# Kernel tuning notes

Hardware: AMD Instinct MI355X
Metric: run time of the kernel (lower is better)

## Reference

```python
import jax, jax.numpy as jnp
import numpy as np

N, L, S, D = 2, 4800, 4800, 256
H0, W0, H1, W1 = 60, 80, 60, 80  # hw0_c, hw1_c (L = H0*W0, S = H1*W1)
THR = 0.2
TEMP = 0.1           # dsmax_temperature
BORDER = 2           # border_rm
INF = 1e9


def setup_inputs() -> dict:
    key = jax.random.key(0)
    k0, k1, k2, k3 = jax.random.split(key, 4)
    feat_c0 = jax.random.normal(k0, (N, L, D), jnp.float32)
    feat_c1 = jax.random.normal(k1, (N, S, D), jnp.float32)
    # final_proj params (Linear(256, 256, bias=True)); scaled like typical init
    W = jax.random.normal(k2, (D, D), jnp.float32) / np.sqrt(D)
    b = jax.random.normal(k3, (D,), jnp.float32) * 0.01
    mask_c0 = jnp.ones((N, L), dtype=bool)
    mask_c1 = jnp.ones((N, S), dtype=bool)
    return {"feat_c0": feat_c0, "feat_c1": feat_c1, "W": W, "b": b,
            "mask_c0": mask_c0, "mask_c1": mask_c1}


def _border_valid(h, w, bd):
    # flattened (h*w,) bool: True away from all four borders (mask_border with v=False)
    r = jnp.arange(h * w)
    hh, ww = r // w, r % w
    return (hh >= bd) & (hh < h - bd) & (ww >= bd) & (ww < w - bd)


def reference(feat_c0, feat_c1, W, b, mask_c0, mask_c1):
    inv_sqrt_d = 1.0 / jnp.sqrt(jnp.asarray(D, jnp.float32))
    # final_proj + 1/sqrt(C) scaling
    f0 = (feat_c0 @ W.T + b) * inv_sqrt_d   # [N, L, D]
    f1 = (feat_c1 @ W.T + b) * inv_sqrt_d   # [N, S, D]
    # pairwise similarity / temperature, masked_fill(-INF) on padded pairs
    sim = jnp.einsum('nlc,nsc->nls', f0, f1) / TEMP   # [N, L, S]
    valid = mask_c0[:, :, None] & mask_c1[:, None, :]
    sim = jnp.where(valid, sim, -INF)
    # dual softmax
    conf_0_to_1 = jax.nn.softmax(sim, axis=2)
    conf_1_to_0 = jax.nn.softmax(sim, axis=1)
    # mutual nearest-neighbour + threshold mask
    m01 = (conf_0_to_1 > THR) & (conf_0_to_1 == conf_0_to_1.max(axis=2, keepdims=True))
    m10 = (conf_1_to_0 > THR) & (conf_1_to_0 == conf_1_to_0.max(axis=1, keepdims=True))
    match_mask = m01 | m10
    # border removal (mask_border with v=False on the [b,h0,w0,h1,w1] view)
    match_mask = (match_mask
                  & _border_valid(H0, W0, BORDER)[None, :, None]
                  & _border_valid(H1, W1, BORDER)[None, None, :])
    # dense form of mconf = max(conf01, conf10) at selected matches
    mconf = jnp.maximum(conf_0_to_1, conf_1_to_0) * match_mask
    return conf_0_to_1, conf_1_to_0, match_mask, mconf
```

## Files before the change

### kernel.cpp

```cpp
#include <hip/hip_runtime.h>

#define LL   4800
#define SSZ  4800
#define DD   256
#define LP   4864
#define NBAT 2

typedef __bf16 bf16x8 __attribute__((ext_vector_type(8)));
typedef float  f32x4  __attribute__((ext_vector_type(4)));

__device__ __forceinline__ unsigned short f2bf(float x) {
  unsigned u = __float_as_uint(x);
  u += 0x7FFFu + ((u >> 16) & 1u);
  return (unsigned short)(u >> 16);
}
__device__ __forceinline__ float bf2f(unsigned short h) {
  return __uint_as_float(((unsigned)h) << 16);
}
__device__ __forceinline__ void gl_lds16(const void* g, void* lds) {
  __builtin_amdgcn_global_load_lds(
      (const __attribute__((address_space(1))) void*)g,
      (__attribute__((address_space(3))) void*)lds, 16, 0, 0);
}
__device__ __forceinline__ bool border_ok(int idx) {
  const int h = idx / 80, w = idx % 80;
  return (h >= 2) && (h < 58) && (w >= 2) && (w < 78);
}
__device__ __forceinline__ void sim_block_decode(int wgid, int& bxs, int& byl, int& bz) {
  const int logical = (wgid & 7) * 361 + (wgid >> 3);
  bz = logical / 1444;
  const int rem = logical - bz * 1444;
  byl = rem / 38;
  bxs = rem - byl * 38;
}

#define F4_FEAT 614400
#define F4_TOT  (F4_FEAT * 2 + 16384)
__global__ void k_convert_all(const float* __restrict__ f0, const float* __restrict__ f1,
                              const float* __restrict__ Wm,
                              unsigned short* __restrict__ fc0hi, unsigned short* __restrict__ fc0lo,
                              unsigned short* __restrict__ fc1hi, unsigned short* __restrict__ fc1lo,
                              unsigned short* __restrict__ Whi,  unsigned short* __restrict__ Wlo) {
  int i = blockIdx.x * blockDim.x + threadIdx.x;
  if (i >= F4_TOT) return;
  const float* src;
  unsigned short *hi, *lo;
  int off;
  if (i < F4_FEAT)          { src = f0; hi = fc0hi; lo = fc0lo; off = i; }
  else if (i < 2 * F4_FEAT) { src = f1; hi = fc1hi; lo = fc1lo; off = i - F4_FEAT; }
  else                      { src = Wm; hi = Whi;  lo = Wlo;  off = i - 2 * F4_FEAT; }
  float4 v = reinterpret_cast<const float4*>(src)[off];
  float xs[4] = {v.x, v.y, v.z, v.w};
  unsigned short hs[4], ls[4];
#pragma unroll
  for (int j = 0; j < 4; ++j) {
    unsigned short h = f2bf(xs[j]);
    hs[j] = h;
    ls[j] = f2bf(xs[j] - bf2f(h));
  }
  ushort4 ho; ho.x = hs[0]; ho.y = hs[1]; ho.z = hs[2]; ho.w = hs[3];
  ushort4 lov; lov.x = ls[0]; lov.y = ls[1]; lov.z = ls[2]; lov.w = ls[3];
  reinterpret_cast<ushort4*>(hi)[off] = ho;
  reinterpret_cast<ushort4*>(lo)[off] = lov;
}

__global__ __launch_bounds__(256, 2)
void k_gemm_proj(const unsigned short* __restrict__ fc0hi, const unsigned short* __restrict__ fc0lo,
                 const unsigned short* __restrict__ fc1hi, const unsigned short* __restrict__ fc1lo,
                 const unsigned short* __restrict__ Whi,  const unsigned short* __restrict__ Wlo,
                 const float* __restrict__ bias,
                 unsigned short* __restrict__ f0h, unsigned short* __restrict__ f1h) {
  extern __shared__ unsigned char smem[];
  unsigned char* sAhi = smem;
  unsigned char* sAlo = smem + 16384;
  unsigned char* sBhi = smem + 32768;
  unsigned char* sBlo = smem + 49152;

  const int t = threadIdx.x;
  const int lane = t & 63, wave = t >> 6;
  const int wr = wave >> 1, wc = wave & 1;
  const int l15 = lane & 15, g4 = lane >> 4;
  const int tr = t >> 3, tch = t & 7;
  const int chg = tch ^ (tr & 7);

  const int mtile = blockIdx.x, ntile = blockIdx.y, tz = blockIdx.z;
  const int nb = (mtile >= 38) ? 1 : 0;
  const int ltile = mtile - nb * 38;

  const unsigned short* Fhi = tz ? fc1hi : fc0hi;
  const unsigned short* Flo = tz ? fc1lo : fc0lo;
  unsigned short* Oh = tz ? f1h : f0h;

  f32x4 acc[4][4] = {};

  for (int kt = 0; kt < DD / 64; ++kt) {
#pragma unroll
    for (int i = 0; i < 4; ++i) {
      const int r = i * 32 + tr;
      const int lrow = ltile * 128 + r;
      const int srcRow = nb * LL + min(lrow, LL - 1);
      const size_t aoff = (size_t)srcRow * DD + kt * 64 + chg * 8;
      const size_t boff = (size_t)(ntile * 128 + r) * DD + kt * 64 + chg * 8;
      const int ldsoff = i * 4096 + t * 16;
      gl_lds16(Fhi + aoff, sAhi + ldsoff);
      gl_lds16(Flo + aoff, sAlo + ldsoff);
      gl_lds16(Whi + boff, sBhi + ldsoff);
      gl_lds16(Wlo + boff, sBlo + ldsoff);
    }
    __syncthreads();
#pragma unroll
    for (int kk = 0; kk < 2; ++kk) {
      bf16x8 ah[4], al[4], bh[4], bl[4];
#pragma unroll
      for (int m = 0; m < 4; ++m) {
        const int r = wr * 64 + m * 16 + l15;
        const int off = r * 128 + (((kk * 4 + g4) ^ (r & 7)) * 16);
        ah[m] = *reinterpret_cast<const bf16x8*>(sAhi + off);
        al[m] = *reinterpret_cast<const bf16x8*>(sAlo + off);
      }
#pragma unroll
      for (int n = 0; n < 4; ++n) {
        const int r = wc * 64 + n * 16 + l15;
        const int off = r * 128 + (((kk * 4 + g4) ^ (r & 7)) * 16);
        bh[n] = *reinterpret_cast<const bf16x8*>(sBhi + off);
        bl[n] = *reinterpret_cast<const bf16x8*>(sBlo + off);
      }
#pragma unroll
      for (int m = 0; m < 4; ++m)
#pragma unroll
        for (int n = 0; n < 4; ++n) {
          acc[m][n] = __builtin_amdgcn_mfma_f32_16x16x32_bf16(ah[m], bh[n], acc[m][n], 0, 0, 0);
          acc[m][n] = __builtin_amdgcn_mfma_f32_16x16x32_bf16(ah[m], bl[n], acc[m][n], 0, 0, 0);
          acc[m][n] = __builtin_amdgcn_mfma_f32_16x16x32_bf16(al[m], bh[n], acc[m][n], 0, 0, 0);
        }
    }
    __syncthreads();
  }

#pragma unroll
  for (int m = 0; m < 4; ++m) {
#pragma unroll
    for (int j = 0; j < 4; ++j) {
      const int lrow = ltile * 128 + wr * 64 + m * 16 + g4 * 4 + j;
      const bool v = lrow < LL;
#pragma unroll
      for (int n = 0; n < 4; ++n) {
        const int dcol = ntile * 128 + wc * 64 + n * 16 + l15;
        float val = v ? (acc[m][n][j] + bias[dcol]) * 0.0625f : 0.0f;
        size_t oi = ((size_t)(nb * LP + lrow)) * DD + dcol;
        Oh[oi] = f2bf(val);
      }
    }
  }
}

__device__ __forceinline__ void sim_gemm(const unsigned short* __restrict__ Ah,
                                         const unsigned short* __restrict__ Bh,
                                         int bxs, int byl,
                                         unsigned char* sA, unsigned char* sB,
                                         f32x4 acc[4][4]) {
  const int t = threadIdx.x;
  const int lane = t & 63, wave = t >> 6;
  const int wr = wave >> 1, wc = wave & 1;
  const int l15 = lane & 15, g4 = lane >> 4;
  const int tr = t >> 3, tch = t & 7;
  const int chg = tch ^ (tr & 7);

  for (int kt = 0; kt < DD / 64; ++kt) {
#pragma unroll
    for (int i = 0; i < 4; ++i) {
      const int r = i * 32 + tr;
      const size_t aoff = (size_t)(byl * 128 + r) * DD + kt * 64 + chg * 8;
      const size_t boff = (size_t)(bxs * 128 + r) * DD + kt * 64 + chg * 8;
      const int ldsoff = i * 4096 + t * 16;
      gl_lds16(Ah + aoff, sA + ldsoff);
      gl_lds16(Bh + boff, sB + ldsoff);
    }
    __syncthreads();
#pragma unroll
    for (int kk = 0; kk < 2; ++kk) {
      bf16x8 ah[4], bh[4];
#pragma unroll
      for (int m = 0; m < 4; ++m) {
        const int r = wr * 64 + m * 16 + l15;
        const int off = r * 128 + (((kk * 4 + g4) ^ (r & 7)) * 16);
        ah[m] = *reinterpret_cast<const bf16x8*>(sA + off);
      }
#pragma unroll
      for (int n = 0; n < 4; ++n) {
        const int r = wc * 64 + n * 16 + l15;
        const int off = r * 128 + (((kk * 4 + g4) ^ (r & 7)) * 16);
        bh[n] = *reinterpret_cast<const bf16x8*>(sB + off);
      }
#pragma unroll
      for (int m = 0; m < 4; ++m)
#pragma unroll
        for (int n = 0; n < 4; ++n)
          acc[m][n] = __builtin_amdgcn_mfma_f32_16x16x32_bf16(ah[m], bh[n], acc[m][n], 0, 0, 0);
    }
    __syncthreads();
  }
}

__global__ __launch_bounds__(256, 2)
void k_sim_stats(const unsigned short* __restrict__ f0h, const unsigned short* __restrict__ f1h,
                 float* __restrict__ rowsum, float* __restrict__ colsum,
                 unsigned* __restrict__ rowmaxU, unsigned* __restrict__ colmaxU) {
  extern __shared__ unsigned char smem[];
  unsigned char* sA = smem;
  unsigned char* sB = smem + 16384;

  const int t = threadIdx.x;
  const int lane = t & 63, wave = t >> 6;
  const int wr = wave >> 1, wc = wave & 1;
  const int l15 = lane & 15, g4 = lane >> 4;

  int bxs, byl, bz;
  sim_block_decode(blockIdx.x, bxs, byl, bz);
  const unsigned short* Ah = f0h + (size_t)bz * LP * DD;
  const unsigned short* Bh = f1h + (size_t)bz * LP * DD;

  f32x4 acc[4][4] = {};
  sim_gemm(Ah, Bh, bxs, byl, sA, sB, acc);

  bool colv[4];
#pragma unroll
  for (int n = 0; n < 4; ++n)
    colv[n] = (bxs * 128 + wc * 64 + n * 16 + l15) < SSZ;

#pragma unroll
  for (int m = 0; m < 4; ++m) {
#pragma unroll
    for (int j = 0; j < 4; ++j) {
      const int lg = byl * 128 + wr * 64 + m * 16 + g4 * 4 + j;
      const bool rowv = lg < LL;
#pragma unroll
      for (int n = 0; n < 4; ++n) {
        float p = __expf(acc[m][n][j] * 10.0f);
        if (!rowv || !colv[n]) p = 0.0f;
        acc[m][n][j] = p;
      }
    }
  }

  float* srow = (float*)smem;
  float* scol = srow + 128;
  unsigned* srm = (unsigned*)(scol + 128);
  unsigned* scm = srm + 128;
  __syncthreads();
  if (t < 128) { srow[t] = 0.f; scol[t] = 0.f; srm[t] = 0u; scm[t] = 0u; }
  __syncthreads();

#pragma unroll
  for (int m = 0; m < 4; ++m) {
#pragma unroll
    for (int j = 0; j < 4; ++j) {
      float s  = acc[m][0][j] + acc[m][1][j] + acc[m][2][j] + acc[m][3][j];
      float mx = fmaxf(fmaxf(acc[m][0][j], acc[m][1][j]), fmaxf(acc[m][2][j], acc[m][3][j]));
#pragma unroll
      for (int o = 1; o < 16; o <<= 1) {
        s += __shfl_xor(s, o);
        mx = fmaxf(mx, __shfl_xor(mx, o));
      }
      if (l15 == 0) {
        const int r = wr * 64 + m * 16 + g4 * 4 + j;
        atomicAdd(&srow[r], s);
        atomicMax(&srm[r], __float_as_uint(mx));
      }
    }
  }
#pragma unroll
  for (int n = 0; n < 4; ++n) {
    float s = 0.f, mx = 0.f;
#pragma unroll
    for (int m = 0; m < 4; ++m)
#pragma unroll
      for (int j = 0; j < 4; ++j) { s += acc[m][n][j]; mx = fmaxf(mx, acc[m][n][j]); }
    s += __shfl_xor(s, 16); mx = fmaxf(mx, __shfl_xor(mx, 16));
    s += __shfl_xor(s, 32); mx = fmaxf(mx, __shfl_xor(mx, 32));
    if (g4 == 0) {
      const int c = wc * 64 + n * 16 + l15;
      atomicAdd(&scol[c], s);
      atomicMax(&scm[c], __float_as_uint(mx));
    }
  }
  __syncthreads();

  if (t < 128) {
    const int lg = byl * 128 + t;
    if (lg < LL) {
      atomicAdd(&rowsum[bz * LL + lg], srow[t]);
      atomicMax(&rowmaxU[bz * LL + lg], srm[t]);
    }
    const int sg = bxs * 128 + t;
    if (sg < SSZ) {
      atomicAdd(&colsum[bz * SSZ + sg], scol[t]);
      atomicMax(&colmaxU[bz * SSZ + sg], scm[t]);
    }
  }
}

__global__ __launch_bounds__(256, 2)
void k_sim_write(const unsigned short* __restrict__ f0h, const unsigned short* __restrict__ f1h,
                 const float* __restrict__ rowsum, const float* __restrict__ colsum,
                 const unsigned* __restrict__ rowmaxU, const unsigned* __restrict__ colmaxU,
                 float* __restrict__ out0, float* __restrict__ out1,
                 float* __restrict__ out2, float* __restrict__ out3) {
  extern __shared__ unsigned char smem[];
  unsigned char* sA = smem;
  unsigned char* sB = smem + 16384;

  const int t = threadIdx.x;
  const int lane = t & 63, wave = t >> 6;
  const int wr = wave >> 1, wc = wave & 1;
  const int l15 = lane & 15, g4 = lane >> 4;

  int bxs, byl, bz;
  sim_block_decode(blockIdx.x, bxs, byl, bz);
  const unsigned short* Ah = f0h + (size_t)bz * LP * DD;
  const unsigned short* Bh = f1h + (size_t)bz * LP * DD;

  f32x4 acc[4][4] = {};
  sim_gemm(Ah, Bh, bxs, byl, sA, sB, acc);

#pragma unroll
  for (int m = 0; m < 4; ++m)
#pragma unroll
    for (int n = 0; n < 4; ++n)
#pragma unroll
      for (int j = 0; j < 4; ++j)
        acc[m][n][j] = __expf(acc[m][n][j] * 10.0f);

  float invrs[16], rpm[16];
  bool  blr[16];
#pragma unroll
  for (int m = 0; m < 4; ++m)
#pragma unroll
    for (int j = 0; j < 4; ++j) {
      const int lg = byl * 128 + wr * 64 + m * 16 + g4 * 4 + j;
      const int lc = min(lg, LL - 1);
      invrs[m * 4 + j] = 1.0f / rowsum[bz * LL + lc];
      rpm[m * 4 + j]   = __uint_as_float(rowmaxU[bz * LL + lc]);
      blr[m * 4 + j]   = border_ok(lc);
    }
  float invcs[4], cpm[4];
  bool  bsc[4];
#pragma unroll
  for (int n = 0; n < 4; ++n) {
    const int sg = bxs * 128 + wc * 64 + n * 16 + l15;
    const int sc = min(sg, SSZ - 1);
    invcs[n] = 1.0f / colsum[bz * SSZ + sc];
    cpm[n]   = __uint_as_float(colmaxU[bz * SSZ + sc]);
    bsc[n]   = border_ok(sc);
  }

  float* sw = (float*)(smem + wave * 8192);
  const int base_row = byl * 128 + wr * 64;
  const int base_col = bxs * 128 + wc * 64;
  float* outs[4] = {out0, out1, out2, out3};

#pragma unroll
  for (int o = 0; o < 4; ++o) {
#pragma unroll
    for (int m = 0; m < 4; ++m) {
#pragma unroll
      for (int j = 0; j < 4; ++j) {
        const int r = 4 * g4 + j;
        const float ir = invrs[m * 4 + j];
        const float rm = rpm[m * 4 + j];
        const bool  bl = blr[m * 4 + j];
#pragma unroll
        for (int n = 0; n < 4; ++n) {
          const float p = acc[m][n][j];
          float val;
          if (o == 0) {
            val = p * ir;
          } else if (o == 1) {
            val = p * invcs[n];
          } else {
            const float c01 = p * ir;
            const float c10 = p * invcs[n];
            const bool m01 = (c01 > 0.2f) && (p >= rm);
            const bool m10 = (c10 > 0.2f) && (p >= cpm[n]);
            const bool mm  = (m01 || m10) && bl && bsc[n];
            val = (o == 2) ? (mm ? 1.0f : 0.0f)
                           : (mm ? fmaxf(c01, c10) : 0.0f);
          }
          sw[r * 68 + n * 16 + l15] = val;
        }
      }
#pragma unroll
      for (int it = 0; it < 4; ++it) {
        const int rr = it * 4 + (lane >> 4);
        const int ch = lane & 15;
        f32x4 v = *reinterpret_cast<const f32x4*>(&sw[rr * 68 + ch * 4]);
        const int grow = base_row + m * 16 + rr;
        const int gcol = base_col + ch * 4;
        if (grow < LL && gcol < SSZ) {
          __builtin_nontemporal_store(
              v, reinterpret_cast<f32x4*>(&outs[o][((size_t)bz * LL + grow) * SSZ + gcol]));
        }
      }
    }
  }
}

extern "C" void kernel_launch(void* const* d_in, const int* in_sizes, int n_in,
                              void* d_out, int out_size, void* d_ws, size_t ws_size,
                              hipStream_t stream) {
  const float* feat0 = (const float*)d_in[0];
  const float* feat1 = (const float*)d_in[1];
  const float* Wm    = (const float*)d_in[2];
  const float* bv    = (const float*)d_in[3];

  char* ws = (char*)d_ws;
  unsigned short* fc0hi = (unsigned short*)(ws + 0);
  unsigned short* fc0lo = (unsigned short*)(ws + 4915200);
  unsigned short* fc1hi = (unsigned short*)(ws + 9830400);
  unsigned short* fc1lo = (unsigned short*)(ws + 14745600);
  unsigned short* Whi   = (unsigned short*)(ws + 19660800);
  unsigned short* Wlo   = (unsigned short*)(ws + 19791872);
  unsigned short* f0h   = (unsigned short*)(ws + 19922944);
  unsigned short* f1h   = (unsigned short*)(ws + 24903680);
  char* statsBase = ws + 29884416;
  float*    rowsum  = (float*)(statsBase + 0);
  float*    colsum  = (float*)(statsBase + 38400);
  unsigned* rowmaxU = (unsigned*)(statsBase + 76800);
  unsigned* colmaxU = (unsigned*)(statsBase + 115200);

  const size_t NLS = (size_t)NBAT * LL * SSZ;
  float* out0 = (float*)d_out;
  float* out1 = out0 + NLS;
  float* out2 = out0 + 2 * NLS;
  float* out3 = out0 + 3 * NLS;

  hipMemsetAsync(statsBase, 0, 153600, stream);

  k_convert_all<<<(F4_TOT + 255) / 256, 256, 0, stream>>>(
      feat0, feat1, Wm, fc0hi, fc0lo, fc1hi, fc1lo, Whi, Wlo);

  k_gemm_proj<<<dim3(76, 2, 2), 256, 65536, stream>>>(
      fc0hi, fc0lo, fc1hi, fc1lo, Whi, Wlo, bv, f0h, f1h);

  k_sim_stats<<<2888, 256, 32768, stream>>>(
      f0h, f1h, rowsum, colsum, rowmaxU, colmaxU);

  k_sim_write<<<2888, 256, 32768, stream>>>(
      f0h, f1h, rowsum, colsum, rowmaxU, colmaxU, out0, out1, out2, out3);
}
```

Before: 248.8 us.

## Double-buffer LDS tiles in similarity GEMM to overlap loads with MFMA

Splits shared memory into two stages so the next K-slice of A and B tiles is loaded asynchronously while MFMAs run on the current slice, replacing the load-sync-compute-sync pattern. The dynamic shared memory for both similarity kernels doubles to 64KB. This aims to hide global-to-LDS latency but may reduce the number of resident blocks per CU.

New measurement: 246.7 us. Within noise of the previous version (-0.8%).

```diff
diff --git a/kernel.cpp b/kernel.cpp
--- a/kernel.cpp
+++ b/kernel.cpp
@@ -157,7 +157,7 @@
 __device__ __forceinline__ void sim_gemm(const unsigned short* __restrict__ Ah,
                                          const unsigned short* __restrict__ Bh,
                                          int bxs, int byl,
-                                         unsigned char* sA, unsigned char* sB,
+                                         unsigned char* smem,
                                          f32x4 acc[4][4]) {
   const int t = threadIdx.x;
   const int lane = t & 63, wave = t >> 6;
@@ -166,17 +166,33 @@
   const int tr = t >> 3, tch = t & 7;
   const int chg = tch ^ (tr & 7);
 
-  for (int kt = 0; kt < DD / 64; ++kt) {
-#pragma unroll
-    for (int i = 0; i < 4; ++i) {
-      const int r = i * 32 + tr;
-      const size_t aoff = (size_t)(byl * 128 + r) * DD + kt * 64 + chg * 8;
-      const size_t boff = (size_t)(bxs * 128 + r) * DD + kt * 64 + chg * 8;
-      const int ldsoff = i * 4096 + t * 16;
-      gl_lds16(Ah + aoff, sA + ldsoff);
-      gl_lds16(Bh + boff, sB + ldsoff);
-    }
-    __syncthreads();
+  const unsigned short* Abase = Ah + (size_t)(byl * 128) * DD + chg * 8;
+  const unsigned short* Bbase = Bh + (size_t)(bxs * 128) * DD + chg * 8;
+
+#define SIM_STAGE(buf, kt)                                                    \
+  {                                                                           \
+    unsigned char* sA_ = smem + (buf) * 32768;                                \
+    unsigned char* sB_ = sA_ + 16384;                                         \
+    _Pragma("unroll")                                                         \
+    for (int i = 0; i < 4; ++i) {                                             \
+      const int r = i * 32 + tr;                                              \
+      const int ldsoff = i * 4096 + t * 16;                                   \
+      gl_lds16(Abase + (size_t)r * DD + (kt) * 64, sA_ + ldsoff);             \
+      gl_lds16(Bbase + (size_t)r * DD + (kt) * 64, sB_ + ldsoff);             \
+    }                                                                         \
+  }
+
+  SIM_STAGE(0, 0);
+  asm volatile("s_waitcnt vmcnt(0)" ::: "memory");
+  __builtin_amdgcn_s_barrier();
+
+#pragma unroll
+  for (int kt = 0; kt < 4; ++kt) {
+    const int cur = kt & 1;
+    if (kt < 3) SIM_STAGE(cur ^ 1, kt + 1);
+
+    unsigned char* sA = smem + cur * 32768;
+    unsigned char* sB = sA + 16384;
 #pragma unroll
     for (int kk = 0; kk < 2; ++kk) {
       bf16x8 ah[4], bh[4];
@@ -198,8 +214,10 @@
         for (int n = 0; n < 4; ++n)
           acc[m][n] = __builtin_amdgcn_mfma_f32_16x16x32_bf16(ah[m], bh[n], acc[m][n], 0, 0, 0);
     }
-    __syncthreads();
-  }
+    if (kt < 3) asm volatile("s_waitcnt vmcnt(0)" ::: "memory");
+    __builtin_amdgcn_s_barrier();
+  }
+#undef SIM_STAGE
 }
 
 __global__ __launch_bounds__(256, 2)
@@ -207,8 +225,6 @@
                  float* __restrict__ rowsum, float* __restrict__ colsum,
                  unsigned* __restrict__ rowmaxU, unsigned* __restrict__ colmaxU) {
   extern __shared__ unsigned char smem[];
-  unsigned char* sA = smem;
-  unsigned char* sB = smem + 16384;
 
   const int t = threadIdx.x;
   const int lane = t & 63, wave = t >> 6;
@@ -221,7 +237,7 @@
   const unsigned short* Bh = f1h + (size_t)bz * LP * DD;
 
   f32x4 acc[4][4] = {};
-  sim_gemm(Ah, Bh, bxs, byl, sA, sB, acc);
+  sim_gemm(Ah, Bh, bxs, byl, smem, acc);
 
   bool colv[4];
 #pragma unroll
@@ -307,8 +323,6 @@
                  float* __restrict__ out0, float* __restrict__ out1,
                  float* __restrict__ out2, float* __restrict__ out3) {
   extern __shared__ unsigned char smem[];
-  unsigned char* sA = smem;
-  unsigned char* sB = smem + 16384;
 
   const int t = threadIdx.x;
   const int lane = t & 63, wave = t >> 6;
@@ -321,7 +335,7 @@
   const unsigned short* Bh = f1h + (size_t)bz * LP * DD;
 
   f32x4 acc[4][4] = {};
-  sim_gemm(Ah, Bh, bxs, byl, sA, sB, acc);
+  sim_gemm(Ah, Bh, bxs, byl, smem, acc);
 
 #pragma unroll
   for (int m = 0; m < 4; ++m)
@@ -442,9 +456,9 @@
   k_gemm_proj<<<dim3(76, 2, 2), 256, 65536, stream>>>(
       fc0hi, fc0lo, fc1hi, fc1lo, Whi, Wlo, bv, f0h, f1h);
 
-  k_sim_stats<<<2888, 256, 32768, stream>>>(
+  k_sim_stats<<<2888, 256, 65536, stream>>>(
       f0h, f1h, rowsum, colsum, rowmaxU, colmaxU);
 
-  k_sim_write<<<2888, 256, 32768, stream>>>(
+  k_sim_write<<<2888, 256, 65536, stream>>>(
       f0h, f1h, rowsum, colsum, rowmaxU, colmaxU, out0, out1, out2, out3);
 }
```

## Store bf16 exp tile in stats pass and finalize from buffer instead of recomputing GEMM

Applied to the files above, without the earlier changes.

The stats kernel now also writes the exponentiated similarity tile, rounded to bf16, into a workspace buffer through LDS-staged nontemporal stores. A new elementwise finalize kernel reads that buffer with the row and column stats and writes the four outputs, replacing the second GEMM pass. This trades a recomputed 4800x4800x256 GEMM per batch for about 92 MB of extra write plus read traffic. It is used only when the workspace is large enough, and exp values are now rounded to bf16 on both paths.

Result: slower. 303.5 us (+22.0%).

```diff
diff --git a/kernel.cpp b/kernel.cpp
--- a/kernel.cpp
+++ b/kernel.cpp
@@ -8,6 +8,7 @@
 
 typedef __bf16 bf16x8 __attribute__((ext_vector_type(8)));
 typedef float  f32x4  __attribute__((ext_vector_type(4)));
+typedef unsigned short u16x8 __attribute__((ext_vector_type(8)));
 
 __device__ __forceinline__ unsigned short f2bf(float x) {
   unsigned u = __float_as_uint(x);
@@ -157,8 +158,10 @@
 __device__ __forceinline__ void sim_gemm(const unsigned short* __restrict__ Ah,
                                          const unsigned short* __restrict__ Bh,
                                          int bxs, int byl,
-                                         unsigned char* sA, unsigned char* sB,
+                                         unsigned char* smem,
                                          f32x4 acc[4][4]) {
+  unsigned char* sA = smem;
+  unsigned char* sB = smem + 16384;
   const int t = threadIdx.x;
   const int lane = t & 63, wave = t >> 6;
   const int wr = wave >> 1, wc = wave & 1;
@@ -204,11 +207,10 @@
 
 __global__ __launch_bounds__(256, 2)
 void k_sim_stats(const unsigned short* __restrict__ f0h, const unsigned short* __restrict__ f1h,
+                 unsigned short* __restrict__ pb,
                  float* __restrict__ rowsum, float* __restrict__ colsum,
                  unsigned* __restrict__ rowmaxU, unsigned* __restrict__ colmaxU) {
   extern __shared__ unsigned char smem[];
-  unsigned char* sA = smem;
-  unsigned char* sB = smem + 16384;
 
   const int t = threadIdx.x;
   const int lane = t & 63, wave = t >> 6;
@@ -221,7 +223,7 @@
   const unsigned short* Bh = f1h + (size_t)bz * LP * DD;
 
   f32x4 acc[4][4] = {};
-  sim_gemm(Ah, Bh, bxs, byl, sA, sB, acc);
+  sim_gemm(Ah, Bh, bxs, byl, smem, acc);
 
   bool colv[4];
 #pragma unroll
@@ -238,7 +240,33 @@
       for (int n = 0; n < 4; ++n) {
         float p = __expf(acc[m][n][j] * 10.0f);
         if (!rowv || !colv[n]) p = 0.0f;
-        acc[m][n][j] = p;
+        acc[m][n][j] = bf2f(f2bf(p));
+      }
+    }
+  }
+
+  if (pb != nullptr) {
+    const int base_row = byl * 128 + wr * 64;
+    const int base_col = bxs * 128 + wc * 64;
+    if (base_col + 64 <= SSZ) {
+      unsigned short* swu = (unsigned short*)(smem + wave * 2304);
+#pragma unroll
+      for (int m = 0; m < 4; ++m) {
+#pragma unroll
+        for (int j = 0; j < 4; ++j)
+#pragma unroll
+          for (int n = 0; n < 4; ++n)
+            swu[(g4 * 4 + j) * 72 + n * 16 + l15] = f2bf(acc[m][n][j]);
+#pragma unroll
+        for (int it = 0; it < 2; ++it) {
+          const int idx = it * 64 + lane;
+          const int rr = idx >> 3, ch = idx & 7;
+          u16x8 v = *reinterpret_cast<const u16x8*>(&swu[rr * 72 + ch * 8]);
+          const int grow = base_row + m * 16 + rr;
+          if (grow < LL)
+            __builtin_nontemporal_store(v, reinterpret_cast<u16x8*>(
+                &pb[((size_t)(bz * LL + grow)) * SSZ + base_col + ch * 8]));
+        }
       }
     }
   }
@@ -300,6 +328,59 @@
   }
 }
 
+__global__ void k_finalize(const unsigned short* __restrict__ pb,
+                           const float* __restrict__ rowsum, const unsigned* __restrict__ rowmaxU,
+                           const float* __restrict__ colsum, const unsigned* __restrict__ colmaxU,
+                           float* __restrict__ out0, float* __restrict__ out1,
+                           float* __restrict__ out2, float* __restrict__ out3) {
+  const unsigned total = 9600u * 600u;
+  for (unsigned q = blockIdx.x * 256u + threadIdx.x; q < total; q += gridDim.x * 256u) {
+    const unsigned rowid = q / 600u;
+    const int s0 = (int)(q - rowid * 600u) * 8;
+    const unsigned nb = rowid / 4800u;
+    const int l = (int)(rowid - nb * 4800u);
+
+    const float rs    = rowsum[rowid];
+    const float invrs = 1.0f / rs;
+    const float rpm   = __uint_as_float(rowmaxU[rowid]);
+    const bool  bl    = border_ok(l);
+
+    const int cbase = (int)nb * 4800 + s0;
+    float4 cs0 = *reinterpret_cast<const float4*>(&colsum[cbase]);
+    float4 cs1 = *reinterpret_cast<const float4*>(&colsum[cbase + 4]);
+    uint4  cm0 = *reinterpret_cast<const uint4*>(&colmaxU[cbase]);
+    uint4  cm1 = *reinterpret_cast<const uint4*>(&colmaxU[cbase + 4]);
+    float css[8]    = {cs0.x, cs0.y, cs0.z, cs0.w, cs1.x, cs1.y, cs1.z, cs1.w};
+    unsigned cms[8] = {cm0.x, cm0.y, cm0.z, cm0.w, cm1.x, cm1.y, cm1.z, cm1.w};
+
+    u16x8 pv = *reinterpret_cast<const u16x8*>(&pb[(size_t)rowid * SSZ + s0]);
+
+    float o0[8], o1[8], o2[8], o3[8];
+#pragma unroll
+    for (int j = 0; j < 8; ++j) {
+      const float p   = bf2f(pv[j]);
+      const float c01 = p * invrs;
+      const float c10 = p / css[j];
+      const bool m01 = (c01 > 0.2f) && (p >= rpm);
+      const bool m10 = (c10 > 0.2f) && (p >= __uint_as_float(cms[j]));
+      const bool mm  = (m01 || m10) && bl && border_ok(s0 + j);
+      o0[j] = c01;
+      o1[j] = c10;
+      o2[j] = mm ? 1.0f : 0.0f;
+      o3[j] = mm ? fmaxf(c01, c10) : 0.0f;
+    }
+    const size_t idx = (size_t)rowid * SSZ + s0;
+    f32x4 v;
+#define NT4(arr, out)                                                          \
+    v[0] = arr[0]; v[1] = arr[1]; v[2] = arr[2]; v[3] = arr[3];                \
+    __builtin_nontemporal_store(v, reinterpret_cast<f32x4*>(&out[idx]));       \
+    v[0] = arr[4]; v[1] = arr[5]; v[2] = arr[6]; v[3] = arr[7];                \
+    __builtin_nontemporal_store(v, reinterpret_cast<f32x4*>(&out[idx + 4]));
+    NT4(o0, out0) NT4(o1, out1) NT4(o2, out2) NT4(o3, out3)
+#undef NT4
+  }
+}
+
 __global__ __launch_bounds__(256, 2)
 void k_sim_write(const unsigned short* __restrict__ f0h, const unsigned short* __restrict__ f1h,
                  const float* __restrict__ rowsum, const float* __restrict__ colsum,
@@ -307,8 +388,6 @@
                  float* __restrict__ out0, float* __restrict__ out1,
                  float* __restrict__ out2, float* __restrict__ out3) {
   extern __shared__ unsigned char smem[];
-  unsigned char* sA = smem;
-  unsigned char* sB = smem + 16384;
 
   const int t = threadIdx.x;
   const int lane = t & 63, wave = t >> 6;
@@ -321,7 +400,7 @@
   const unsigned short* Bh = f1h + (size_t)bz * LP * DD;
 
   f32x4 acc[4][4] = {};
-  sim_gemm(Ah, Bh, bxs, byl, sA, sB, acc);
+  sim_gemm(Ah, Bh, bxs, byl, smem, acc);
 
 #pragma unroll
   for (int m = 0; m < 4; ++m)
@@ -329,7 +408,7 @@
     for (int n = 0; n < 4; ++n)
 #pragma unroll
       for (int j = 0; j < 4; ++j)
-        acc[m][n][j] = __expf(acc[m][n][j] * 10.0f);
+        acc[m][n][j] = bf2f(f2bf(__expf(acc[m][n][j] * 10.0f)));
 
   float invrs[16], rpm[16];
   bool  blr[16];
@@ -428,6 +507,11 @@
   unsigned* rowmaxU = (unsigned*)(statsBase + 76800);
   unsigned* colmaxU = (unsigned*)(statsBase + 115200);
 
+  const size_t PB_OFF = 33554432;
+  const size_t PB_BYTES = (size_t)9600 * 4800 * 2;
+  const bool fast = ws_size >= PB_OFF + PB_BYTES;
+  unsigned short* pbBuf = fast ? (unsigned short*)(ws + PB_OFF) : nullptr;
+
   const size_t NLS = (size_t)NBAT * LL * SSZ;
   float* out0 = (float*)d_out;
   float* out1 = out0 + NLS;
@@ -443,8 +527,13 @@
       fc0hi, fc0lo, fc1hi, fc1lo, Whi, Wlo, bv, f0h, f1h);
 
   k_sim_stats<<<2888, 256, 32768, stream>>>(
-      f0h, f1h, rowsum, colsum, rowmaxU, colmaxU);
-
-  k_sim_write<<<2888, 256, 32768, stream>>>(
-      f0h, f1h, rowsum, colsum, rowmaxU, colmaxU, out0, out1, out2, out3);
-}
+      f0h, f1h, pbBuf, rowsum, colsum, rowmaxU, colmaxU);
+
+  if (fast) {
+    k_finalize<<<4096, 256, 0, stream>>>(
+        pbBuf, rowsum, rowmaxU, colsum, colmaxU, out0, out1, out2, out3);
+  } else {
+    k_sim_write<<<2888, 256, 32768, stream>>>(
+        f0h, f1h, rowsum, colsum, rowmaxU, colmaxU, out0, out1, out2, out3);
+  }
+}
```
